# Optimization experiments

Measured on AMD Instinct MI355X. Metric: run time of the kernel, lower is better.

## Reference

```python
import jax, jax.numpy as jnp
import numpy as np

HIDDEN = 768
NUM_HEADS = 12
HEAD_SIZE = HIDDEN // NUM_HEADS
LN_EPS = 1e-5


def setup_inputs() -> dict:
    key = jax.random.key(0)
    ks = jax.random.split(key, 10)
    B, S, H = 2, 4096, HIDDEN
    std = 1.0 / np.sqrt(H)
    inp = {
        "hidden_states": jax.random.normal(ks[0], (B, S, H), dtype=jnp.float32),
        "attention_mask": jnp.ones((B, S), dtype=jnp.float32),
        "Wq": jax.random.normal(ks[1], (H, H), dtype=jnp.float32) * std,
        "bq": jnp.zeros((H,), dtype=jnp.float32),
        "Wk": jax.random.normal(ks[2], (H, H), dtype=jnp.float32) * std,
        "bk": jnp.zeros((H,), dtype=jnp.float32),
        "Wv": jax.random.normal(ks[3], (H, H), dtype=jnp.float32) * std,
        "bv": jnp.zeros((H,), dtype=jnp.float32),
        "Wo": jax.random.normal(ks[4], (H, H), dtype=jnp.float32) * std,
        "bo": jnp.zeros((H,), dtype=jnp.float32),
        "ln_gamma": jnp.ones((H,), dtype=jnp.float32),
        "ln_beta": jnp.zeros((H,), dtype=jnp.float32),
    }
    return inp


def _split_heads(x):
    # [B, S, H] -> [B, nH, S, hd]
    B, S, _ = x.shape
    return x.reshape(B, S, NUM_HEADS, HEAD_SIZE).transpose(0, 2, 1, 3)


def reference(hidden_states, attention_mask, Wq, bq, Wk, bk, Wv, bv, Wo, bo, ln_gamma, ln_beta):
    # QKV projections (torch Linear: x @ W.T + b; here W is stored as [in, out])
    q = _split_heads(hidden_states @ Wq + bq)
    k = _split_heads(hidden_states @ Wk + bk)
    v = _split_heads(hidden_states @ Wv + bv)

    scores = jnp.einsum("bhqd,bhkd->bhqk", q, k) / jnp.sqrt(jnp.float32(HEAD_SIZE))
    # additive mask: (1 - mask) * -10000, broadcast over heads and query positions
    scores = scores + (1.0 - attention_mask)[:, None, None, :] * -10000.0
    probs = jax.nn.softmax(scores, axis=-1)  # dropout_prob = 0 -> identity

    ctx = jnp.einsum("bhqk,bhkd->bhqd", probs, v)
    B, _, S, _ = ctx.shape
    ctx = ctx.transpose(0, 2, 1, 3).reshape(B, S, HIDDEN)

    out = ctx @ Wo + bo
    resid = out + hidden_states
    mu = jnp.mean(resid, axis=-1, keepdims=True)
    var = jnp.var(resid, axis=-1, keepdims=True)
    return (resid - mu) * jax.lax.rsqrt(var + LN_EPS) * ln_gamma + ln_beta
```

## Files before the change

### kernel.cpp

```cpp
#include <hip/hip_runtime.h>
#include <hip/hip_bf16.h>

#define HID 768
#define NHEADS 12
#define HDIM 64
#define SEQ 4096
#define BB 2
#define MTOT (BB * SEQ)

typedef __attribute__((ext_vector_type(8))) short bf16x8;
typedef __attribute__((ext_vector_type(16))) float f32x16;

#define LOG2E 1.4426950408889634f

__device__ inline unsigned pack2bf(float a, float b) {
    __hip_bfloat162 h = __float22bfloat162_rn(float2{a, b});
    return *(unsigned*)&h;
}

__global__ __launch_bounds__(256) void cast_x_kernel(
    const float* __restrict__ X, __hip_bfloat16* __restrict__ Xb)
{
    const size_t i = ((size_t)blockIdx.x * 256 + threadIdx.x) * 8;
    const float4 x0 = *(const float4*)(X + i);
    const float4 x1 = *(const float4*)(X + i + 4);
    unsigned u[4];
    u[0] = pack2bf(x0.x, x0.y);
    u[1] = pack2bf(x0.z, x0.w);
    u[2] = pack2bf(x1.x, x1.y);
    u[3] = pack2bf(x1.z, x1.w);
    *(uint4*)(Xb + i) = *(uint4*)u;
}

__global__ __launch_bounds__(256) void pack_w_kernel(
    const float* __restrict__ Wq, const float* __restrict__ Wk,
    const float* __restrict__ Wv, const float* __restrict__ Wo,
    __hip_bfloat16* __restrict__ Wt)
{
    const int z = blockIdx.z;
    const float* __restrict__ W = (z == 0) ? Wq : (z == 1) ? Wk : (z == 2) ? Wv : Wo;
    const int in0  = blockIdx.x * 64;
    const int out0 = blockIdx.y * 64;
    const int t = threadIdx.x;

    __shared__ float T[64][65];
#pragma unroll
    for (int i = 0; i < 4; ++i) {
        const int idx = t + 256 * i;
        const int row = idx >> 4;
        const int c4  = (idx & 15) << 2;
        const float4 v = *(const float4*)(W + (size_t)(in0 + row) * HID + out0 + c4);
        T[row][c4 + 0] = v.x; T[row][c4 + 1] = v.y;
        T[row][c4 + 2] = v.z; T[row][c4 + 3] = v.w;
    }
    __syncthreads();

    const int o  = t >> 2;
    const int cb = (t & 3) << 4;
    __hip_bfloat16 tmp[16];
#pragma unroll
    for (int k = 0; k < 16; ++k)
        tmp[k] = __float2bfloat16(T[cb + k][o]);
    __hip_bfloat16* __restrict__ dst =
        Wt + (size_t)(z * HID + out0 + o) * HID + in0 + cb;
    *(uint4*)(dst)     = *(uint4*)(&tmp[0]);
    *(uint4*)(dst + 8) = *(uint4*)(&tmp[8]);
}

#define GSTAGE(ASB, BSB, BUF, APTR, BPTR, K0) do {                                 \
    _Pragma("unroll")                                                              \
    for (int j_ = 0; j_ < 4; ++j_) {                                               \
        const __hip_bfloat16* ga_ = (APTR) + (size_t)(r0 + 32 * j_) * HID + (K0) + csw; \
        const __hip_bfloat16* gb_ = (BPTR) + (size_t)(r0 + 32 * j_) * HID + (K0) + csw; \
        __builtin_amdgcn_global_load_lds(                                          \
            (const __attribute__((address_space(1))) unsigned*)ga_,                \
            (__attribute__((address_space(3))) unsigned*)(&ASB[BUF][0][0] + (256 * j_ + 64 * w) * 8), 16, 0, 0); \
        __builtin_amdgcn_global_load_lds(                                          \
            (const __attribute__((address_space(1))) unsigned*)gb_,                \
            (__attribute__((address_space(3))) unsigned*)(&BSB[BUF][0][0] + (256 * j_ + 64 * w) * 8), 16, 0, 0); \
    }                                                                              \
} while (0)

#define GTILE(ASB, BSB, BUF) do {                                                  \
    _Pragma("unroll")                                                              \
    for (int kh = 0; kh < 4; ++kh) {                                               \
        const int sc = ((2 * kh + g) ^ (col & 7)) << 3;                            \
        const bf16x8 a0 = *(const bf16x8*)&ASB[BUF][64 * wm + col][sc];            \
        const bf16x8 a1 = *(const bf16x8*)&ASB[BUF][64 * wm + 32 + col][sc];       \
        const bf16x8 b0 = *(const bf16x8*)&BSB[BUF][64 * wn + col][sc];            \
        const bf16x8 b1 = *(const bf16x8*)&BSB[BUF][64 * wn + 32 + col][sc];       \
        acc[0][0] = __builtin_amdgcn_mfma_f32_32x32x16_bf16(a0, b0, acc[0][0], 0, 0, 0); \
        acc[0][1] = __builtin_amdgcn_mfma_f32_32x32x16_bf16(a0, b1, acc[0][1], 0, 0, 0); \
        acc[1][0] = __builtin_amdgcn_mfma_f32_32x32x16_bf16(a1, b0, acc[1][0], 0, 0, 0); \
        acc[1][1] = __builtin_amdgcn_mfma_f32_32x32x16_bf16(a1, b1, acc[1][1], 0, 0, 0); \
    }                                                                              \
} while (0)

__global__ __launch_bounds__(256) void qkv_mfma_kernel(
    const __hip_bfloat16* __restrict__ Xb, const __hip_bfloat16* __restrict__ Wt,
    const float* __restrict__ bq, const float* __restrict__ bk,
    const float* __restrict__ bv,
    __hip_bfloat16* __restrict__ Qo, __hip_bfloat16* __restrict__ Ko,
    __hip_bfloat16* __restrict__ Vo)
{
    const int nblk = blockIdx.x;
    const int z  = nblk / 6;
    const int f0 = (nblk % 6) * 128;
    const int n0 = nblk * 128;
    const int m0 = blockIdx.y * 128;

    const float* __restrict__ bias = (z == 0) ? bq : (z == 1) ? bk : bv;

    const int t    = threadIdx.x;
    const int w    = t >> 6;
    const int lane = t & 63;
    const int col  = lane & 31;
    const int g    = lane >> 5;
    const int wm   = w & 1;
    const int wn   = w >> 1;

    __shared__ __hip_bfloat16 smem[4 * 128 * 64];
    __hip_bfloat16 (*Asb)[128][64] = (__hip_bfloat16(*)[128][64])smem;
    __hip_bfloat16 (*Bsb)[128][64] = (__hip_bfloat16(*)[128][64])(smem + 2 * 128 * 64);

    const int r0  = t >> 3;
    const int csw = (((t & 7) ^ (r0 & 7)) << 3);

    const __hip_bfloat16* __restrict__ Am = Xb + (size_t)m0 * HID;
    const __hip_bfloat16* __restrict__ Bn = Wt + (size_t)n0 * HID;

    f32x16 acc[2][2];
#pragma unroll
    for (int mt = 0; mt < 2; ++mt)
#pragma unroll
        for (int nt = 0; nt < 2; ++nt)
#pragma unroll
            for (int r = 0; r < 16; ++r) acc[mt][nt][r] = 0.f;

    GSTAGE(Asb, Bsb, 0, Am, Bn, 0);
    __syncthreads();
    for (int k0 = 0; k0 < HID; k0 += 128) {
        GSTAGE(Asb, Bsb, 1, Am, Bn, k0 + 64);
        GTILE(Asb, Bsb, 0);
        __syncthreads();
        if (k0 + 128 < HID) GSTAGE(Asb, Bsb, 0, Am, Bn, k0 + 128);
        GTILE(Asb, Bsb, 1);
        __syncthreads();
    }

    if (z < 2) {
        __hip_bfloat16* __restrict__ Out = (z == 0) ? Qo : Ko;
        const int h = (f0 >> 6) + wn;
#pragma unroll
        for (int mt = 0; mt < 2; ++mt)
#pragma unroll
            for (int nt = 0; nt < 2; ++nt) {
                const int d = 32 * nt + col;
                const float bsv = bias[f0 + 64 * wn + d];
#pragma unroll
                for (int r = 0; r < 16; ++r) {
                    const int m = m0 + 64 * wm + 32 * mt + (r & 3) + 8 * (r >> 2) + 4 * g;
                    const int b = m >> 12;
                    const int s = m & (SEQ - 1);
                    Out[(((size_t)(b * NHEADS + h)) * SEQ + s) * HDIM + d] =
                        __float2bfloat16(acc[mt][nt][r] + bsv);
                }
            }
    } else {
        __syncthreads();
        __hip_bfloat16 (*Ts)[136] = (__hip_bfloat16(*)[136])smem;
#pragma unroll
        for (int mt = 0; mt < 2; ++mt)
#pragma unroll
            for (int nt = 0; nt < 2; ++nt) {
                const int nloc = 64 * wn + 32 * nt + col;
                const float bsv = bias[f0 + nloc];
#pragma unroll
                for (int rg = 0; rg < 4; ++rg) {
                    const int mbase = 64 * wm + 32 * mt + 8 * rg + 4 * g;
                    unsigned pu[2];
                    pu[0] = pack2bf(acc[mt][nt][4 * rg + 0] + bsv,
                                    acc[mt][nt][4 * rg + 1] + bsv);
                    pu[1] = pack2bf(acc[mt][nt][4 * rg + 2] + bsv,
                                    acc[mt][nt][4 * rg + 3] + bsv);
                    *(uint2*)&Ts[nloc][mbase] = *(uint2*)pu;
                }
            }
        __syncthreads();
        const int nloc = t >> 1;
        const int half = t & 1;
        const int hh = (f0 >> 6) + (nloc >> 6);
        const int d  = nloc & 63;
        const int bb = m0 >> 12;
        const int s0 = m0 & (SEQ - 1);
        __hip_bfloat16* __restrict__ dst =
            Vo + (((size_t)(bb * NHEADS + hh)) * HDIM + d) * SEQ + s0 + 64 * half;
        const __hip_bfloat16* srcp = &Ts[nloc][64 * half];
#pragma unroll
        for (int j = 0; j < 8; ++j)
            *(uint4*)(dst + 8 * j) = *(const uint4*)(srcp + 8 * j);
    }
}

typedef __attribute__((ext_vector_type(2))) unsigned uswap2;

__global__ __launch_bounds__(256, 3) void attn_kernel(
    const __hip_bfloat16* __restrict__ Qb, const __hip_bfloat16* __restrict__ Kb,
    const __hip_bfloat16* __restrict__ Vt, const float* __restrict__ mask,
    __hip_bfloat16* __restrict__ Ctx)
{
    const int bh = blockIdx.y;
    const int b  = bh / NHEADS;
    const int h  = bh - b * NHEADS;

    const int t    = threadIdx.x;
    const int w    = t >> 6;
    const int lane = t & 63;
    const int col  = lane & 31;
    const int g    = lane >> 5;
    const int qw   = blockIdx.x * 128 + 32 * w;

    __shared__ __hip_bfloat16 Ksb[2][64][64];
    __shared__ __hip_bfloat16 Vsb[2][64][64];
    __shared__ float madd[SEQ];
    __shared__ float ls[4][32];

    const __hip_bfloat16* __restrict__ Qh = Qb + (size_t)bh * SEQ * HDIM;
    const __hip_bfloat16* __restrict__ Kh = Kb + (size_t)bh * SEQ * HDIM;
    const __hip_bfloat16* __restrict__ Vh = Vt + (size_t)bh * HDIM * SEQ;

    for (int j = t; j < SEQ; j += 256)
        madd[j] = (1.0f - mask[b * SEQ + j]) * (-80000.0f);

    const int r0  = t >> 3;
    const int csw = (((t & 7) ^ (r0 & 7)) << 3);

#define STAGE(BUF, KT) do {                                                        \
    const __hip_bfloat16* gk0_ = Kh + (size_t)((KT) + r0) * HDIM + csw;            \
    const __hip_bfloat16* gk1_ = Kh + (size_t)((KT) + r0 + 32) * HDIM + csw;       \
    const __hip_bfloat16* gv0_ = Vh + (size_t)r0 * SEQ + (KT) + csw;               \
    const __hip_bfloat16* gv1_ = Vh + (size_t)(r0 + 32) * SEQ + (KT) + csw;        \
    __hip_bfloat16* lk_ = &Ksb[BUF][0][0] + w * 512;                               \
    __hip_bfloat16* lv_ = &Vsb[BUF][0][0] + w * 512;                               \
    __builtin_amdgcn_global_load_lds(                                              \
        (const __attribute__((address_space(1))) unsigned*)gk0_,                   \
        (__attribute__((address_space(3))) unsigned*)lk_, 16, 0, 0);               \
    __builtin_amdgcn_global_load_lds(                                              \
        (const __attribute__((address_space(1))) unsigned*)gk1_,                   \
        (__attribute__((address_space(3))) unsigned*)(lk_ + 2048), 16, 0, 0);      \
    __builtin_amdgcn_global_load_lds(                                              \
        (const __attribute__((address_space(1))) unsigned*)gv0_,                   \
        (__attribute__((address_space(3))) unsigned*)lv_, 16, 0, 0);               \
    __builtin_amdgcn_global_load_lds(                                              \
        (const __attribute__((address_space(1))) unsigned*)gv1_,                   \
        (__attribute__((address_space(3))) unsigned*)(lv_ + 2048), 16, 0, 0);      \
} while (0)

    bf16x8 bq[4];
#pragma unroll
    for (int kh = 0; kh < 4; ++kh)
        bq[kh] = *(const bf16x8*)(Qh + (size_t)(qw + col) * HDIM + 16 * kh + 8 * g);

    f32x16 O[2];
    float lac = 0.f;
#pragma unroll
    for (int dt = 0; dt < 2; ++dt)
#pragma unroll
        for (int r = 0; r < 16; ++r) O[dt][r] = 0.f;

    const float kscale = 0.125f * LOG2E;

#define ATTN_TILE(BUF, KT0) do {                                                   \
    f32x16 St[2];                                                                  \
    _Pragma("unroll")                                                              \
    for (int nt = 0; nt < 2; ++nt)                                                 \
        _Pragma("unroll")                                                          \
        for (int b4 = 0; b4 < 4; ++b4) {                                           \
            const float4 mm = *(const float4*)&madd[(KT0) + 32 * nt + 8 * b4 + 4 * g]; \
            St[nt][4 * b4 + 0] = mm.x; St[nt][4 * b4 + 1] = mm.y;                  \
            St[nt][4 * b4 + 2] = mm.z; St[nt][4 * b4 + 3] = mm.w;                  \
        }                                                                          \
    _Pragma("unroll")                                                              \
    for (int kh = 0; kh < 4; ++kh) {                                               \
        const int sc = ((2 * kh + g) ^ (col & 7)) << 3;                            \
        const bf16x8 ak0 = *(const bf16x8*)&Ksb[BUF][col][sc];                     \
        const bf16x8 ak1 = *(const bf16x8*)&Ksb[BUF][32 + col][sc];                \
        St[0] = __builtin_amdgcn_mfma_f32_32x32x16_bf16(ak0, bq[kh], St[0], 0, 0, 0); \
        St[1] = __builtin_amdgcn_mfma_f32_32x32x16_bf16(ak1, bq[kh], St[1], 0, 0, 0); \
    }                                                                              \
    unsigned g4x[2][4], g4y[2][4];                                                 \
    _Pragma("unroll")                                                              \
    for (int nt = 0; nt < 2; ++nt) {                                               \
        _Pragma("unroll")                                                          \
        for (int b4 = 0; b4 < 4; ++b4) {                                           \
            const float p0 = __builtin_amdgcn_exp2f(St[nt][4 * b4 + 0] * kscale);  \
            const float p1 = __builtin_amdgcn_exp2f(St[nt][4 * b4 + 1] * kscale);  \
            const float p2 = __builtin_amdgcn_exp2f(St[nt][4 * b4 + 2] * kscale);  \
            const float p3 = __builtin_amdgcn_exp2f(St[nt][4 * b4 + 3] * kscale);  \
            lac += (p0 + p1) + (p2 + p3);                                          \
            g4x[nt][b4] = pack2bf(p0, p1);                                         \
            g4y[nt][b4] = pack2bf(p2, p3);                                         \
        }                                                                          \
    }                                                                              \
    _Pragma("unroll")                                                              \
    for (int kh = 0; kh < 4; ++kh) {                                               \
        const int nt  = kh >> 1;                                                   \
        const int khl = kh & 1;                                                    \
        union { unsigned u[4]; bf16x8 v; } au;                                     \
        ATTN_PTRANS(au, g4x[nt][2 * khl], g4x[nt][2 * khl + 1],                    \
                        g4y[nt][2 * khl], g4y[nt][2 * khl + 1]);                   \
        const int sc = ((2 * kh + g) ^ (col & 7)) << 3;                            \
        const bf16x8 bv0 = *(const bf16x8*)&Vsb[BUF][col][sc];                     \
        const bf16x8 bv1 = *(const bf16x8*)&Vsb[BUF][32 + col][sc];                \
        O[0] = __builtin_amdgcn_mfma_f32_32x32x16_bf16(au.v, bv0, O[0], 0, 0, 0);  \
        O[1] = __builtin_amdgcn_mfma_f32_32x32x16_bf16(au.v, bv1, O[1], 0, 0, 0);  \
    }                                                                              \
} while (0)

#if __has_builtin(__builtin_amdgcn_permlane32_swap)
#define ATTN_PTRANS(au, lox, hix, loy, hiy) do {                                   \
    uswap2 sx_ = __builtin_amdgcn_permlane32_swap((lox), (hix), false, false);     \
    uswap2 sy_ = __builtin_amdgcn_permlane32_swap((loy), (hiy), false, false);     \
    au.u[0] = sx_[0]; au.u[1] = sy_[0]; au.u[2] = sx_[1]; au.u[3] = sy_[1];        \
} while (0)
#else
#define ATTN_PTRANS(au, lox, hix, loy, hiy) do {                                   \
    const unsigned sxv_ = g ? (lox) : (hix);                                       \
    const unsigned syv_ = g ? (loy) : (hiy);                                       \
    const unsigned rx_ = (unsigned)__shfl_xor((int)sxv_, 32, 64);                  \
    const unsigned ry_ = (unsigned)__shfl_xor((int)syv_, 32, 64);                  \
    if (g) { au.u[0] = rx_;   au.u[1] = ry_;   au.u[2] = (hix); au.u[3] = (hiy); } \
    else   { au.u[0] = (lox); au.u[1] = (loy); au.u[2] = rx_;   au.u[3] = ry_;  }  \
} while (0)
#endif

    STAGE(0, 0);
    __syncthreads();

    for (int kt0 = 0; kt0 < SEQ; kt0 += 128) {
        STAGE(1, kt0 + 64);
        ATTN_TILE(0, kt0);
        __syncthreads();
        if (kt0 + 128 < SEQ) STAGE(0, kt0 + 128);
        ATTN_TILE(1, kt0 + 64);
        __syncthreads();
    }
#undef STAGE
#undef ATTN_TILE
#undef ATTN_PTRANS

    {
        const float l = lac + __shfl_xor(lac, 32, 64);
        if (g == 0) ls[w][col] = 1.0f / l;
#pragma unroll
        for (int r = 0; r < 16; ++r) {
            const int qloc = (r & 3) + 8 * (r >> 2) + 4 * g;
            const float inv = ls[w][qloc];
            const int q = qw + qloc;
#pragma unroll
            for (int dt = 0; dt < 2; ++dt) {
                const int d = 32 * dt + col;
                Ctx[((size_t)b * SEQ + q) * HID + h * HDIM + d] =
                    __float2bfloat16(O[dt][r] * inv);
            }
        }
    }
}

__global__ __launch_bounds__(256) void out_mfma_kernel(
    const __hip_bfloat16* __restrict__ Cb, const __hip_bfloat16* __restrict__ Wto,
    const float* __restrict__ bo, const float* __restrict__ X,
    float* __restrict__ Resid)
{
    const int n0 = blockIdx.x * 128;
    const int m0 = blockIdx.y * 128;

    const int t    = threadIdx.x;
    const int w    = t >> 6;
    const int lane = t & 63;
    const int col  = lane & 31;
    const int g    = lane >> 5;
    const int wm   = w & 1;
    const int wn   = w >> 1;

    __shared__ __hip_bfloat16 smem[4 * 128 * 64];
    __hip_bfloat16 (*Asb)[128][64] = (__hip_bfloat16(*)[128][64])smem;
    __hip_bfloat16 (*Bsb)[128][64] = (__hip_bfloat16(*)[128][64])(smem + 2 * 128 * 64);

    const int r0  = t >> 3;
    const int csw = (((t & 7) ^ (r0 & 7)) << 3);

    const __hip_bfloat16* __restrict__ Am = Cb  + (size_t)m0 * HID;
    const __hip_bfloat16* __restrict__ Bn = Wto + (size_t)n0 * HID;

    f32x16 acc[2][2];
#pragma unroll
    for (int mt = 0; mt < 2; ++mt)
#pragma unroll
        for (int nt = 0; nt < 2; ++nt)
#pragma unroll
            for (int r = 0; r < 16; ++r) acc[mt][nt][r] = 0.f;

    GSTAGE(Asb, Bsb, 0, Am, Bn, 0);
    __syncthreads();
    for (int k0 = 0; k0 < HID; k0 += 128) {
        GSTAGE(Asb, Bsb, 1, Am, Bn, k0 + 64);
        GTILE(Asb, Bsb, 0);
        __syncthreads();
        if (k0 + 128 < HID) GSTAGE(Asb, Bsb, 0, Am, Bn, k0 + 128);
        GTILE(Asb, Bsb, 1);
        __syncthreads();
    }

#pragma unroll
    for (int mt = 0; mt < 2; ++mt)
#pragma unroll
        for (int nt = 0; nt < 2; ++nt) {
            const int n = n0 + 64 * wn + 32 * nt + col;
            const float bsv = bo[n];
#pragma unroll
            for (int r = 0; r < 16; ++r) {
                const int m = m0 + 64 * wm + 32 * mt + (r & 3) + 8 * (r >> 2) + 4 * g;
                Resid[(size_t)m * HID + n] = acc[mt][nt][r] + bsv + X[(size_t)m * HID + n];
            }
        }
}

__global__ __launch_bounds__(256) void ln_kernel(
    const float* __restrict__ Rin, const float* __restrict__ gamma,
    const float* __restrict__ beta, float* __restrict__ Out)
{
    const int row = blockIdx.x;
    const int t   = threadIdx.x;
    const float* __restrict__ x = Rin + (size_t)row * HID;

    const float v0 = x[t];
    const float v1 = x[t + 256];
    const float v2 = x[t + 512];
    float s  = v0 + v1 + v2;
    float s2 = v0 * v0 + v1 * v1 + v2 * v2;
#pragma unroll
    for (int off = 32; off; off >>= 1) {
        s  += __shfl_xor(s,  off, 64);
        s2 += __shfl_xor(s2, off, 64);
    }
    __shared__ float rs[4], rs2[4];
    const int w = t >> 6, lane = t & 63;
    if (lane == 0) { rs[w] = s; rs2[w] = s2; }
    __syncthreads();
    const float tot  = rs[0] + rs[1] + rs[2] + rs[3];
    const float tot2 = rs2[0] + rs2[1] + rs2[2] + rs2[3];
    const float mu   = tot * (1.0f / HID);
    const float var  = tot2 * (1.0f / HID) - mu * mu;
    const float rsig = rsqrtf(var + 1e-5f);

    float* __restrict__ y = Out + (size_t)row * HID;
    y[t]       = (v0 - mu) * rsig * gamma[t]       + beta[t];
    y[t + 256] = (v1 - mu) * rsig * gamma[t + 256] + beta[t + 256];
    y[t + 512] = (v2 - mu) * rsig * gamma[t + 512] + beta[t + 512];
}

extern "C" void kernel_launch(void* const* d_in, const int* in_sizes, int n_in,
                              void* d_out, int out_size, void* d_ws, size_t ws_size,
                              hipStream_t stream)
{
    const float* X     = (const float*)d_in[0];
    const float* mask  = (const float*)d_in[1];
    const float* Wq    = (const float*)d_in[2];
    const float* bq    = (const float*)d_in[3];
    const float* Wk    = (const float*)d_in[4];
    const float* bk    = (const float*)d_in[5];
    const float* Wv    = (const float*)d_in[6];
    const float* bv    = (const float*)d_in[7];
    const float* Wo    = (const float*)d_in[8];
    const float* bo    = (const float*)d_in[9];
    const float* gamma = (const float*)d_in[10];
    const float* beta  = (const float*)d_in[11];
    float* out = (float*)d_out;

    const size_t N = (size_t)MTOT * HID;
    const size_t WTE = (size_t)4 * HID * HID;

    char* p = (char*)d_ws;
    __hip_bfloat16* Xb  = (__hip_bfloat16*)p;  p += 2 * N;
    __hip_bfloat16* Wt  = (__hip_bfloat16*)p;  p += 2 * WTE;
    __hip_bfloat16* Qw  = (__hip_bfloat16*)p;  p += 2 * N;
    __hip_bfloat16* Kw  = (__hip_bfloat16*)p;  p += 2 * N;
    __hip_bfloat16* Vtw = (__hip_bfloat16*)p;  p += 2 * N;

    __hip_bfloat16* Ctxb = Xb;
    float* Rd = (float*)Kw;

    cast_x_kernel<<<(int)(N / 2048), 256, 0, stream>>>(X, Xb);
    pack_w_kernel<<<dim3(12, 12, 4), 256, 0, stream>>>(Wq, Wk, Wv, Wo, Wt);
    qkv_mfma_kernel<<<dim3(18, MTOT / 128), 256, 0, stream>>>(
        Xb, Wt, bq, bk, bv, Qw, Kw, Vtw);
    attn_kernel<<<dim3(SEQ / 128, BB * NHEADS), 256, 0, stream>>>(
        Qw, Kw, Vtw, mask, Ctxb);
    out_mfma_kernel<<<dim3(6, MTOT / 128), 256, 0, stream>>>(
        Ctxb, Wt + (size_t)2304 * HID, bo, X, Rd);
    ln_kernel<<<MTOT, 256, 0, stream>>>(Rd, gamma, beta, out);
}
```

Baseline: 324.1 us.

## Fold softmax scale into Q projection and compute row sums via MFMA

The softmax scale (1/sqrt(d)·log2e) moves into the Q projection epilogue, which removes a per-element multiply before exp2 in the attention inner loop, and the mask constant is rescaled to match. The per-thread scalar accumulation of softmax denominators is replaced by an extra MFMA against a ones vector, so row sums come out in the same layout as O. That drops the final cross-lane shuffle and shared-memory pass. The cost is a third MFMA per k-step (50% more PV MFMA work) and the sum is now taken over bf16-rounded probabilities, which changes numerics slightly.

```diff
diff --git a/kernel.cpp b/kernel.cpp
--- a/kernel.cpp
+++ b/kernel.cpp
@@ -12,6 +12,7 @@
 typedef __attribute__((ext_vector_type(16))) float f32x16;
 
 #define LOG2E 1.4426950408889634f
+#define KSCALE (0.125f * LOG2E)
 
 __device__ inline unsigned pack2bf(float a, float b) {
     __hip_bfloat162 h = __float22bfloat162_rn(float2{a, b});
@@ -150,6 +151,7 @@
 
     if (z < 2) {
         __hip_bfloat16* __restrict__ Out = (z == 0) ? Qo : Ko;
+        const float qscale = (z == 0) ? KSCALE : 1.0f;
         const int h = (f0 >> 6) + wn;
 #pragma unroll
         for (int mt = 0; mt < 2; ++mt)
@@ -163,7 +165,7 @@
                     const int b = m >> 12;
                     const int s = m & (SEQ - 1);
                     Out[(((size_t)(b * NHEADS + h)) * SEQ + s) * HDIM + d] =
-                        __float2bfloat16(acc[mt][nt][r] + bsv);
+                        __float2bfloat16((acc[mt][nt][r] + bsv) * qscale);
                 }
             }
     } else {
@@ -223,14 +225,13 @@
     __shared__ __hip_bfloat16 Ksb[2][64][64];
     __shared__ __hip_bfloat16 Vsb[2][64][64];
     __shared__ float madd[SEQ];
-    __shared__ float ls[4][32];
 
     const __hip_bfloat16* __restrict__ Qh = Qb + (size_t)bh * SEQ * HDIM;
     const __hip_bfloat16* __restrict__ Kh = Kb + (size_t)bh * SEQ * HDIM;
     const __hip_bfloat16* __restrict__ Vh = Vt + (size_t)bh * HDIM * SEQ;
 
     for (int j = t; j < SEQ; j += 256)
-        madd[j] = (1.0f - mask[b * SEQ + j]) * (-80000.0f);
+        madd[j] = (1.0f - mask[b * SEQ + j]) * (-10000.0f * LOG2E);
 
     const int r0  = t >> 3;
     const int csw = (((t & 7) ^ (r0 & 7)) << 3);
@@ -261,14 +262,18 @@
     for (int kh = 0; kh < 4; ++kh)
         bq[kh] = *(const bf16x8*)(Qh + (size_t)(qw + col) * HDIM + 16 * kh + 8 * g);
 
-    f32x16 O[2];
-    float lac = 0.f;
+    union { unsigned u[4]; bf16x8 v; } on_;
+    on_.u[0] = 0x3F803F80u; on_.u[1] = 0x3F803F80u;
+    on_.u[2] = 0x3F803F80u; on_.u[3] = 0x3F803F80u;
+    const bf16x8 vones = on_.v;
+
+    f32x16 O[2], Osum;
 #pragma unroll
     for (int dt = 0; dt < 2; ++dt)
 #pragma unroll
         for (int r = 0; r < 16; ++r) O[dt][r] = 0.f;
-
-    const float kscale = 0.125f * LOG2E;
+#pragma unroll
+    for (int r = 0; r < 16; ++r) Osum[r] = 0.f;
 
 #define ATTN_TILE(BUF, KT0) do {                                                   \
     f32x16 St[2];                                                                  \
@@ -293,11 +298,10 @@
     for (int nt = 0; nt < 2; ++nt) {                                               \
         _Pragma("unroll")                                                          \
         for (int b4 = 0; b4 < 4; ++b4) {                                           \
-            const float p0 = __builtin_amdgcn_exp2f(St[nt][4 * b4 + 0] * kscale);  \
-            const float p1 = __builtin_amdgcn_exp2f(St[nt][4 * b4 + 1] * kscale);  \
-            const float p2 = __builtin_amdgcn_exp2f(St[nt][4 * b4 + 2] * kscale);  \
-            const float p3 = __builtin_amdgcn_exp2f(St[nt][4 * b4 + 3] * kscale);  \
-            lac += (p0 + p1) + (p2 + p3);                                          \
+            const float p0 = __builtin_amdgcn_exp2f(St[nt][4 * b4 + 0]);           \
+            const float p1 = __builtin_amdgcn_exp2f(St[nt][4 * b4 + 1]);           \
+            const float p2 = __builtin_amdgcn_exp2f(St[nt][4 * b4 + 2]);           \
+            const float p3 = __builtin_amdgcn_exp2f(St[nt][4 * b4 + 3]);           \
             g4x[nt][b4] = pack2bf(p0, p1);                                         \
             g4y[nt][b4] = pack2bf(p2, p3);                                         \
         }                                                                          \
@@ -312,8 +316,9 @@
         const int sc = ((2 * kh + g) ^ (col & 7)) << 3;                            \
         const bf16x8 bv0 = *(const bf16x8*)&Vsb[BUF][col][sc];                     \
         const bf16x8 bv1 = *(const bf16x8*)&Vsb[BUF][32 + col][sc];                \
-        O[0] = __builtin_amdgcn_mfma_f32_32x32x16_bf16(au.v, bv0, O[0], 0, 0, 0);  \
-        O[1] = __builtin_amdgcn_mfma_f32_32x32x16_bf16(au.v, bv1, O[1], 0, 0, 0);  \
+        O[0]  = __builtin_amdgcn_mfma_f32_32x32x16_bf16(au.v, bv0, O[0], 0, 0, 0); \
+        O[1]  = __builtin_amdgcn_mfma_f32_32x32x16_bf16(au.v, bv1, O[1], 0, 0, 0); \
+        Osum  = __builtin_amdgcn_mfma_f32_32x32x16_bf16(au.v, vones, Osum, 0, 0, 0); \
     }                                                                              \
 } while (0)
 
@@ -349,20 +354,16 @@
 #undef ATTN_TILE
 #undef ATTN_PTRANS
 
-    {
-        const float l = lac + __shfl_xor(lac, 32, 64);
-        if (g == 0) ls[w][col] = 1.0f / l;
-#pragma unroll
-        for (int r = 0; r < 16; ++r) {
-            const int qloc = (r & 3) + 8 * (r >> 2) + 4 * g;
-            const float inv = ls[w][qloc];
-            const int q = qw + qloc;
-#pragma unroll
-            for (int dt = 0; dt < 2; ++dt) {
-                const int d = 32 * dt + col;
-                Ctx[((size_t)b * SEQ + q) * HID + h * HDIM + d] =
-                    __float2bfloat16(O[dt][r] * inv);
-            }
+#pragma unroll
+    for (int r = 0; r < 16; ++r) {
+        const int qloc = (r & 3) + 8 * (r >> 2) + 4 * g;
+        const float inv = 1.0f / Osum[r];
+        const int q = qw + qloc;
+#pragma unroll
+        for (int dt = 0; dt < 2; ++dt) {
+            const int d = 32 * dt + col;
+            Ctx[((size_t)b * SEQ + q) * HID + h * HDIM + d] =
+                __float2bfloat16(O[dt][r] * inv);
         }
     }
 }
```

Result: faster. 307.1 us (-5.3%).
